# Performance work log

Measured on AMD Instinct MI355X. Metric: run time of the kernel, lower is better.

The kernel has to match this reference:

```python
import jax, jax.numpy as jnp
import numpy as np

N_EMBD = 1024
N_HEAD = 16

def setup_inputs() -> dict:
    key = jax.random.key(0)
    k1, k2, k3 = jax.random.split(key, 3)
    x = jax.random.normal(k1, (2, 2048, N_EMBD), dtype=jnp.float32)
    # torch Linear(n, 3n): y = x @ W_attn (we store transposed weight directly)
    w_attn = jax.random.normal(k2, (N_EMBD, 3 * N_EMBD), dtype=jnp.float32) * 0.02
    w_proj = jax.random.normal(k3, (N_EMBD, N_EMBD), dtype=jnp.float32) * 0.02
    return {"x": x, "w_attn": w_attn, "w_proj": w_proj}

def reference(x, w_attn, w_proj):
    B, S, E = x.shape
    H = N_HEAD
    D = E // H
    qkv = x @ w_attn  # [B, S, 3E]
    q, k, v = jnp.split(qkv, 3, axis=-1)
    # [B, H, S, D]
    q = q.reshape(B, S, H, D).transpose(0, 2, 1, 3)
    k = k.reshape(B, S, H, D).transpose(0, 2, 1, 3)
    v = v.reshape(B, S, H, D).transpose(0, 2, 1, 3)
    scale = 1.0 / jnp.sqrt(jnp.asarray(D, dtype=x.dtype))
    a = jnp.einsum('bhqd,bhkd->bhqk', q, k) * scale  # [B, H, S, S]
    causal = jnp.tril(jnp.ones((S, S), dtype=bool))
    a = jnp.where(causal, a, -jnp.inf)
    a = jax.nn.softmax(a, axis=-1)
    y = jnp.einsum('bhqk,bhkd->bhqd', a, v)  # [B, H, S, D]
    y = y.transpose(0, 2, 1, 3).reshape(B, S, E)
    return y @ w_proj
```

## Files before the change

### kernel.cpp

```cpp
#include <hip/hip_runtime.h>

#define DEVI __device__ __forceinline__

typedef short bf16x8 __attribute__((ext_vector_type(8)));
typedef float f32x4 __attribute__((ext_vector_type(4)));
typedef unsigned short u16;
typedef unsigned int u32;

static constexpr int Bn = 2, S = 2048, E = 1024, H = 16, D = 64;
static constexpr int Mrows = Bn * S;
static constexpr int N_QKV = 3 * E;

DEVI u16 f2b(float f) {
  union { float f; u32 u; } c; c.f = f;
  return (u16)((c.u + 0x7FFFu + ((c.u >> 16) & 1u)) >> 16);
}

DEVI bf16x8 ld8(const u16* p) {
  union { uint4 u; bf16x8 v; } c;
  c.u = *reinterpret_cast<const uint4*>(p);
  return c.v;
}

#define MFMA(a, b, c) __builtin_amdgcn_mfma_f32_16x16x32_bf16(a, b, c, 0, 0, 0)

#define G2L16(gptr, lptr) \
  __builtin_amdgcn_global_load_lds((const __attribute__((address_space(1))) void*)(gptr), \
                                   (__attribute__((address_space(3))) void*)(lptr), 16, 0, 0)

__global__ void conv_bf16(const float* __restrict__ in, u16* __restrict__ out, int n4) {
  int i = blockIdx.x * blockDim.x + threadIdx.x;
  if (i < n4) {
    float4 f = reinterpret_cast<const float4*>(in)[i];
    ushort4 u;
    u.x = f2b(f.x); u.y = f2b(f.y); u.z = f2b(f.z); u.w = f2b(f.w);
    reinterpret_cast<ushort4*>(out)[i] = u;
  }
}

__global__ void transpose_bf16(const float* __restrict__ in, u16* __restrict__ out, int R, int C) {
  __shared__ float t[32][33];
  int bx = blockIdx.x * 32;
  int by = blockIdx.y * 32;
  int tx = threadIdx.x, ty = threadIdx.y;
#pragma unroll
  for (int k = 0; k < 32; k += 8)
    t[ty + k][tx] = in[(size_t)(by + ty + k) * C + bx + tx];
  __syncthreads();
#pragma unroll
  for (int k = 0; k < 32; k += 8)
    out[(size_t)(bx + ty + k) * R + by + tx] = f2b(t[tx][ty + k]);
}

__global__ __launch_bounds__(256) void gemm_qkv(const u16* __restrict__ A, const u16* __restrict__ BT,
                                                u16* __restrict__ Qb, u16* __restrict__ Kb,
                                                u16* __restrict__ VbT) {
  constexpr int K = 1024, BK = 64;
  __shared__ __align__(16) u16 As[128 * BK];
  __shared__ __align__(16) u16 Bs[128 * BK];
  int tid = threadIdx.x;
  int w = tid >> 6, lane = tid & 63, quad = lane >> 4, l15 = lane & 15;
  int m0 = blockIdx.x * 128, n0 = blockIdx.y * 128;
  int mw = (w >> 1) * 64, nw = (w & 1) * 64;
  const u16* Ab = A + (size_t)m0 * K;
  const u16* Bb = BT + (size_t)n0 * K;
  f32x4 acc[4][4] = {};
  for (int k0 = 0; k0 < K; k0 += BK) {
#pragma unroll
    for (int j = 0; j < 4; j++) {
      int L = j * 256 + tid;
      int row = L >> 3, cg = (L & 7) ^ (row & 7);
      G2L16(Ab + (size_t)row * K + k0 + cg * 8, (char*)As + L * 16);
    }
#pragma unroll
    for (int j = 0; j < 4; j++) {
      int L = j * 256 + tid;
      int row = L >> 3, cg = (L & 7) ^ (row & 7);
      G2L16(Bb + (size_t)row * K + k0 + cg * 8, (char*)Bs + L * 16);
    }
    __syncthreads();
#pragma unroll
    for (int kk = 0; kk < 2; kk++) {
      int sg = ((kk << 2) | quad) ^ (l15 & 7);
      bf16x8 a[4], b[4];
#pragma unroll
      for (int i = 0; i < 4; i++) a[i] = ld8(&As[(mw + i * 16 + l15) * BK + sg * 8]);
#pragma unroll
      for (int i = 0; i < 4; i++) b[i] = ld8(&Bs[(nw + i * 16 + l15) * BK + sg * 8]);
#pragma unroll
      for (int mb = 0; mb < 4; mb++)
#pragma unroll
        for (int nb = 0; nb < 4; nb++)
          acc[mb][nb] = MFMA(a[mb], b[nb], acc[mb][nb]);
    }
    __syncthreads();
  }
#pragma unroll
  for (int mb = 0; mb < 4; mb++) {
    int m = m0 + mw + mb * 16 + quad * 4;
    int b = m >> 11, s = m & 2047;
#pragma unroll
    for (int nb = 0; nb < 4; nb++) {
      int n = n0 + nw + nb * 16 + l15;
      int sec = n >> 10, e = n & 1023, h = e >> 6, d = e & 63;
      int bh = b * H + h;
      if (sec == 0) {
#pragma unroll
        for (int r = 0; r < 4; r++)
          Qb[((size_t)bh * S + s + r) * D + d] = f2b(acc[mb][nb][r] * 0.125f);
      } else if (sec == 1) {
#pragma unroll
        for (int r = 0; r < 4; r++)
          Kb[((size_t)bh * S + s + r) * D + d] = f2b(acc[mb][nb][r]);
      } else {
        ushort4 v;
        v.x = f2b(acc[mb][nb][0]); v.y = f2b(acc[mb][nb][1]);
        v.z = f2b(acc[mb][nb][2]); v.w = f2b(acc[mb][nb][3]);
        *reinterpret_cast<ushort4*>(VbT + ((size_t)bh * D + d) * S + s) = v;
      }
    }
  }
}

__global__ __launch_bounds__(256, 3) void attn(const u16* __restrict__ Qb, const u16* __restrict__ Kb,
                                               const u16* __restrict__ VbT, u16* __restrict__ Yb) {
  __shared__ __align__(16) u16 Ks[128 * 64];
  __shared__ __align__(16) u16 Vs[64 * 128];
  __shared__ __align__(16) u32 Ps[4][16 * 68];
  int w = threadIdx.x >> 6, lane = threadIdx.x & 63, quad = lane >> 4, l15 = lane & 15;
  int bh = blockIdx.x & 31, p = blockIdx.x >> 5;
  int b = bh >> 4, h = bh & 15;

  const u16* Kbh = Kb + (size_t)bh * S * D;
  const u16* Vbh = VbT + (size_t)bh * D * S;
  u32* myP = &Ps[w][0];
  const u16* myP16 = (const u16*)myP;
  int prow = l15 * 68 + quad * 2;

#pragma unroll 1
  for (int ph = 0; ph < 2; ph++) {
    int qt = ph ? p : 31 - p;
    int q_base = qt * 64 + w * 16;
    int qrow = q_base + l15;
    int kmax = q_base + 16;
    int kend = (qt + 1) * 64;

    const u16* Qp = Qb + ((size_t)bh * S + qrow) * D + quad * 8;
    bf16x8 bq0 = ld8(Qp), bq1 = ld8(Qp + 32);

    float lpart = 0.f;
    f32x4 o[4] = {};

    for (int kbase = 0; kbase < kend; kbase += 128) {
      __syncthreads();
      const u16* Kg = Kbh + (size_t)kbase * D;
#pragma unroll
      for (int j = 0; j < 4; j++) {
        int L = (w * 4 + j) * 64 + lane;
        int row = L >> 3, cg = (L & 7) ^ (row & 7);
        G2L16(Kg + (size_t)row * 64 + cg * 8, (char*)Ks + L * 16);
      }
      const u16* Vg = Vbh + kbase;
#pragma unroll
      for (int j = 0; j < 4; j++) {
        int L = (w * 4 + j) * 64 + lane;
        int row = L >> 4, cg = (L & 15) ^ (row & 15);
        G2L16(Vg + (size_t)row * S + cg * 8, (char*)Vs + L * 16);
      }
      __syncthreads();

#pragma unroll
      for (int mb = 0; mb < 8; mb++) {
        int kb = kbase + mb * 16;
        u32 pa = 0, pb = 0;
        if (kb < kmax) {
          int row = mb * 16 + l15;
          bf16x8 ak0 = ld8(&Ks[row * 64 + ((quad ^ (row & 7)) * 8)]);
          bf16x8 ak1 = ld8(&Ks[row * 64 + (((quad + 4) ^ (row & 7)) * 8)]);
          f32x4 z = {};
          z = MFMA(ak0, bq0, z);
          z = MFMA(ak1, bq1, z);
          if (kb == q_base) {
#pragma unroll
            for (int r = 0; r < 4; r++)
              if (quad * 4 + r > l15) z[r] = -1e30f;
          }
          float p0 = __expf(z[0]), p1 = __expf(z[1]);
          float p2 = __expf(z[2]), p3 = __expf(z[3]);
          lpart += (p0 + p1) + (p2 + p3);
          pa = (u32)f2b(p0) | ((u32)f2b(p1) << 16);
          pb = (u32)f2b(p2) | ((u32)f2b(p3) << 16);
        }
        uint2 pw; pw.x = pa; pw.y = pb;
        *reinterpret_cast<uint2*>(&myP[prow + mb * 8]) = pw;
      }
#pragma unroll
      for (int ch = 0; ch < 4; ch++) {
        if (kbase + ch * 32 < kmax) {
          bf16x8 bp = ld8(myP16 + l15 * 136 + ch * 32 + quad * 8);
#pragma unroll
          for (int dd = 0; dd < 4; dd++) {
            int rv = dd * 16 + l15;
            bf16x8 av = ld8(&Vs[rv * 128 + (((ch * 4 + quad) ^ (rv & 15)) * 8)]);
            o[dd] = MFMA(av, bp, o[dd]);
          }
        }
      }
    }

    float l = lpart;
    l += __shfl_xor(l, 16);
    l += __shfl_xor(l, 32);
    float rinv = 1.0f / l;
    u16* Yp = Yb + ((size_t)b * S + qrow) * E + h * 64 + quad * 4;
#pragma unroll
    for (int dd = 0; dd < 4; dd++) {
      ushort4 y;
      y.x = f2b(o[dd][0] * rinv); y.y = f2b(o[dd][1] * rinv);
      y.z = f2b(o[dd][2] * rinv); y.w = f2b(o[dd][3] * rinv);
      *reinterpret_cast<ushort4*>(Yp + dd * 16) = y;
    }
  }
}

__global__ __launch_bounds__(256) void gemm_proj(const u16* __restrict__ A, const u16* __restrict__ BT,
                                                 float* __restrict__ out) {
  constexpr int K = 1024, BK = 64;
  __shared__ __align__(16) u16 As[128 * BK];
  __shared__ __align__(16) u16 Bs[128 * BK];
  int tid = threadIdx.x;
  int w = tid >> 6, lane = tid & 63, quad = lane >> 4, l15 = lane & 15;
  int m0 = blockIdx.x * 128, n0 = blockIdx.y * 128;
  int mw = (w >> 1) * 64, nw = (w & 1) * 64;
  const u16* Ab = A + (size_t)m0 * K;
  const u16* Bb = BT + (size_t)n0 * K;
  f32x4 acc[4][4] = {};
  for (int k0 = 0; k0 < K; k0 += BK) {
#pragma unroll
    for (int j = 0; j < 4; j++) {
      int L = j * 256 + tid;
      int row = L >> 3, cg = (L & 7) ^ (row & 7);
      G2L16(Ab + (size_t)row * K + k0 + cg * 8, (char*)As + L * 16);
    }
#pragma unroll
    for (int j = 0; j < 4; j++) {
      int L = j * 256 + tid;
      int row = L >> 3, cg = (L & 7) ^ (row & 7);
      G2L16(Bb + (size_t)row * K + k0 + cg * 8, (char*)Bs + L * 16);
    }
    __syncthreads();
#pragma unroll
    for (int kk = 0; kk < 2; kk++) {
      int sg = ((kk << 2) | quad) ^ (l15 & 7);
      bf16x8 a[4], b[4];
#pragma unroll
      for (int i = 0; i < 4; i++) a[i] = ld8(&As[(mw + i * 16 + l15) * BK + sg * 8]);
#pragma unroll
      for (int i = 0; i < 4; i++) b[i] = ld8(&Bs[(nw + i * 16 + l15) * BK + sg * 8]);
#pragma unroll
      for (int mb = 0; mb < 4; mb++)
#pragma unroll
        for (int nb = 0; nb < 4; nb++)
          acc[mb][nb] = MFMA(a[mb], b[nb], acc[mb][nb]);
    }
    __syncthreads();
  }
#pragma unroll
  for (int mb = 0; mb < 4; mb++) {
    int m = m0 + mw + mb * 16 + quad * 4;
#pragma unroll
    for (int nb = 0; nb < 4; nb++) {
      int n = n0 + nw + nb * 16 + l15;
#pragma unroll
      for (int r = 0; r < 4; r++)
        out[(size_t)(m + r) * E + n] = acc[mb][nb][r];
    }
  }
}

extern "C" void kernel_launch(void* const* d_in, const int* in_sizes, int n_in,
                              void* d_out, int out_size, void* d_ws, size_t ws_size,
                              hipStream_t stream) {
  const float* x = (const float*)d_in[0];
  const float* w_attn = (const float*)d_in[1];
  const float* w_proj = (const float*)d_in[2];
  float* out = (float*)d_out;
  char* ws = (char*)d_ws;

  u16* xb   = (u16*)(ws);
  u16* wabT = (u16*)(ws + 8388608);
  u16* wpbT = (u16*)(ws + 14680064);
  u16* Qb   = (u16*)(ws + 16777216);
  u16* Kb   = (u16*)(ws + 25165824);
  u16* VbT  = (u16*)(ws + 33554432);
  u16* Yb   = (u16*)(ws + 41943040);

  conv_bf16<<<4096, 256, 0, stream>>>(x, xb, Mrows * E / 4);
  transpose_bf16<<<dim3(N_QKV / 32, E / 32), dim3(32, 8), 0, stream>>>(w_attn, wabT, E, N_QKV);
  transpose_bf16<<<dim3(E / 32, E / 32), dim3(32, 8), 0, stream>>>(w_proj, wpbT, E, E);
  gemm_qkv<<<dim3(Mrows / 128, N_QKV / 128), 256, 0, stream>>>(xb, wabT, Qb, Kb, VbT);
  attn<<<Bn * H * (S / 128), 256, 0, stream>>>(Qb, Kb, VbT, Yb);
  gemm_proj<<<dim3(Mrows / 128, E / 128), 256, 0, stream>>>(Yb, wpbT, out);
}
```

Measured before the change: 188.7 us.

## Load GEMM B operand directly from global and fuse paired attention query tiles

```diff
diff --git a/kernel.cpp b/kernel.cpp
--- a/kernel.cpp
+++ b/kernel.cpp
@@ -55,38 +55,32 @@
 __global__ __launch_bounds__(256) void gemm_qkv(const u16* __restrict__ A, const u16* __restrict__ BT,
                                                 u16* __restrict__ Qb, u16* __restrict__ Kb,
                                                 u16* __restrict__ VbT) {
-  constexpr int K = 1024, BK = 64;
+  constexpr int K = 1024, BK = 128;
   __shared__ __align__(16) u16 As[128 * BK];
-  __shared__ __align__(16) u16 Bs[128 * BK];
   int tid = threadIdx.x;
   int w = tid >> 6, lane = tid & 63, quad = lane >> 4, l15 = lane & 15;
   int m0 = blockIdx.x * 128, n0 = blockIdx.y * 128;
   int mw = (w >> 1) * 64, nw = (w & 1) * 64;
   const u16* Ab = A + (size_t)m0 * K;
-  const u16* Bb = BT + (size_t)n0 * K;
+  const u16* Bp = BT + (size_t)(n0 + nw + l15) * K + quad * 8;
   f32x4 acc[4][4] = {};
   for (int k0 = 0; k0 < K; k0 += BK) {
 #pragma unroll
-    for (int j = 0; j < 4; j++) {
+    for (int j = 0; j < 8; j++) {
       int L = j * 256 + tid;
-      int row = L >> 3, cg = (L & 7) ^ (row & 7);
+      int row = L >> 4, cg = (L & 15) ^ (row & 15);
       G2L16(Ab + (size_t)row * K + k0 + cg * 8, (char*)As + L * 16);
     }
-#pragma unroll
-    for (int j = 0; j < 4; j++) {
-      int L = j * 256 + tid;
-      int row = L >> 3, cg = (L & 7) ^ (row & 7);
-      G2L16(Bb + (size_t)row * K + k0 + cg * 8, (char*)Bs + L * 16);
-    }
-    __syncthreads();
-#pragma unroll
-    for (int kk = 0; kk < 2; kk++) {
-      int sg = ((kk << 2) | quad) ^ (l15 & 7);
-      bf16x8 a[4], b[4];
-#pragma unroll
-      for (int i = 0; i < 4; i++) a[i] = ld8(&As[(mw + i * 16 + l15) * BK + sg * 8]);
-#pragma unroll
-      for (int i = 0; i < 4; i++) b[i] = ld8(&Bs[(nw + i * 16 + l15) * BK + sg * 8]);
+    __syncthreads();
+#pragma unroll
+    for (int kk = 0; kk < 4; kk++) {
+      bf16x8 b[4];
+#pragma unroll
+      for (int nb = 0; nb < 4; nb++) b[nb] = ld8(Bp + (size_t)nb * 16 * K + k0 + kk * 32);
+      bf16x8 a[4];
+#pragma unroll
+      for (int i = 0; i < 4; i++)
+        a[i] = ld8(&As[(mw + i * 16 + l15) * BK + ((((kk << 2) | quad) ^ l15) * 8)]);
 #pragma unroll
       for (int mb = 0; mb < 4; mb++)
 #pragma unroll
@@ -130,6 +124,8 @@
   int w = threadIdx.x >> 6, lane = threadIdx.x & 63, quad = lane >> 4, l15 = lane & 15;
   int bh = blockIdx.x & 31, p = blockIdx.x >> 5;
   int b = bh >> 4, h = bh & 15;
+  int qtA = 31 - p, qtB = p;
+  int ncA = (qtA + 2) >> 1, ncB = (qtB + 2) >> 1;
 
   const u16* Kbh = Kb + (size_t)bh * S * D;
   const u16* Vbh = VbT + (size_t)bh * D * S;
@@ -137,87 +133,102 @@
   const u16* myP16 = (const u16*)myP;
   int prow = l15 * 68 + quad * 2;
 
-#pragma unroll 1
-  for (int ph = 0; ph < 2; ph++) {
-    int qt = ph ? p : 31 - p;
-    int q_base = qt * 64 + w * 16;
-    int qrow = q_base + l15;
-    int kmax = q_base + 16;
-    int kend = (qt + 1) * 64;
-
-    const u16* Qp = Qb + ((size_t)bh * S + qrow) * D + quad * 8;
-    bf16x8 bq0 = ld8(Qp), bq1 = ld8(Qp + 32);
-
-    float lpart = 0.f;
-    f32x4 o[4] = {};
-
-    for (int kbase = 0; kbase < kend; kbase += 128) {
-      __syncthreads();
-      const u16* Kg = Kbh + (size_t)kbase * D;
-#pragma unroll
-      for (int j = 0; j < 4; j++) {
-        int L = (w * 4 + j) * 64 + lane;
-        int row = L >> 3, cg = (L & 7) ^ (row & 7);
-        G2L16(Kg + (size_t)row * 64 + cg * 8, (char*)Ks + L * 16);
+  int qbA = qtA * 64 + w * 16, qbB = qtB * 64 + w * 16;
+  int kmaxA = qbA + 16, kmaxB = qbB + 16;
+  const u16* QpA = Qb + ((size_t)bh * S + qbA + l15) * D + quad * 8;
+  const u16* QpB = Qb + ((size_t)bh * S + qbB + l15) * D + quad * 8;
+  bf16x8 bqA0 = ld8(QpA), bqA1 = ld8(QpA + 32);
+  bf16x8 bqB0 = ld8(QpB), bqB1 = ld8(QpB + 32);
+
+  float lA = 0.f, lB = 0.f;
+  f32x4 oA[4] = {}, oB[4] = {};
+  int kbase = 0;
+
+  auto process = [&](int q_base, int kmaxW, bf16x8 bq0, bf16x8 bq1, f32x4* o, float& lpart) {
+#pragma unroll
+    for (int mb = 0; mb < 8; mb++) {
+      int kb = kbase + mb * 16;
+      u32 pa = 0, pb = 0;
+      if (kb < kmaxW) {
+        int row = mb * 16 + l15;
+        bf16x8 ak0 = ld8(&Ks[row * 64 + ((quad ^ (row & 7)) * 8)]);
+        bf16x8 ak1 = ld8(&Ks[row * 64 + (((quad + 4) ^ (row & 7)) * 8)]);
+        f32x4 z = {};
+        z = MFMA(ak0, bq0, z);
+        z = MFMA(ak1, bq1, z);
+        if (kb == q_base) {
+#pragma unroll
+          for (int r = 0; r < 4; r++)
+            if (quad * 4 + r > l15) z[r] = -1e30f;
+        }
+        float p0 = __expf(z[0]), p1 = __expf(z[1]);
+        float p2 = __expf(z[2]), p3 = __expf(z[3]);
+        lpart += (p0 + p1) + (p2 + p3);
+        pa = (u32)f2b(p0) | ((u32)f2b(p1) << 16);
+        pb = (u32)f2b(p2) | ((u32)f2b(p3) << 16);
       }
-      const u16* Vg = Vbh + kbase;
-#pragma unroll
-      for (int j = 0; j < 4; j++) {
-        int L = (w * 4 + j) * 64 + lane;
-        int row = L >> 4, cg = (L & 15) ^ (row & 15);
-        G2L16(Vg + (size_t)row * S + cg * 8, (char*)Vs + L * 16);
-      }
-      __syncthreads();
-
-#pragma unroll
-      for (int mb = 0; mb < 8; mb++) {
-        int kb = kbase + mb * 16;
-        u32 pa = 0, pb = 0;
-        if (kb < kmax) {
-          int row = mb * 16 + l15;
-          bf16x8 ak0 = ld8(&Ks[row * 64 + ((quad ^ (row & 7)) * 8)]);
-          bf16x8 ak1 = ld8(&Ks[row * 64 + (((quad + 4) ^ (row & 7)) * 8)]);
-          f32x4 z = {};
-          z = MFMA(ak0, bq0, z);
-          z = MFMA(ak1, bq1, z);
-          if (kb == q_base) {
-#pragma unroll
-            for (int r = 0; r < 4; r++)
-              if (quad * 4 + r > l15) z[r] = -1e30f;
-          }
-          float p0 = __expf(z[0]), p1 = __expf(z[1]);
-          float p2 = __expf(z[2]), p3 = __expf(z[3]);
-          lpart += (p0 + p1) + (p2 + p3);
-          pa = (u32)f2b(p0) | ((u32)f2b(p1) << 16);
-          pb = (u32)f2b(p2) | ((u32)f2b(p3) << 16);
-        }
-        uint2 pw; pw.x = pa; pw.y = pb;
-        *reinterpret_cast<uint2*>(&myP[prow + mb * 8]) = pw;
-      }
-#pragma unroll
-      for (int ch = 0; ch < 4; ch++) {
-        if (kbase + ch * 32 < kmax) {
-          bf16x8 bp = ld8(myP16 + l15 * 136 + ch * 32 + quad * 8);
-#pragma unroll
-          for (int dd = 0; dd < 4; dd++) {
-            int rv = dd * 16 + l15;
-            bf16x8 av = ld8(&Vs[rv * 128 + (((ch * 4 + quad) ^ (rv & 15)) * 8)]);
-            o[dd] = MFMA(av, bp, o[dd]);
-          }
+      uint2 pw; pw.x = pa; pw.y = pb;
+      *reinterpret_cast<uint2*>(&myP[prow + mb * 8]) = pw;
+    }
+#pragma unroll
+    for (int ch = 0; ch < 4; ch++) {
+      if (kbase + ch * 32 < kmaxW) {
+        bf16x8 bp = ld8(myP16 + l15 * 136 + ch * 32 + quad * 8);
+#pragma unroll
+        for (int dd = 0; dd < 4; dd++) {
+          int rv = dd * 16 + l15;
+          bf16x8 av = ld8(&Vs[rv * 128 + (((ch * 4 + quad) ^ (rv & 15)) * 8)]);
+          o[dd] = MFMA(av, bp, o[dd]);
         }
       }
     }
-
-    float l = lpart;
-    l += __shfl_xor(l, 16);
-    l += __shfl_xor(l, 32);
+  };
+
+  for (int c = 0; c < ncA; c++) {
+    kbase = c * 128;
+    __syncthreads();
+    const u16* Kg = Kbh + (size_t)kbase * D;
+#pragma unroll
+    for (int j = 0; j < 4; j++) {
+      int L = (w * 4 + j) * 64 + lane;
+      int row = L >> 3, cg = (L & 7) ^ (row & 7);
+      G2L16(Kg + (size_t)row * 64 + cg * 8, (char*)Ks + L * 16);
+    }
+    const u16* Vg = Vbh + kbase;
+#pragma unroll
+    for (int j = 0; j < 4; j++) {
+      int L = (w * 4 + j) * 64 + lane;
+      int row = L >> 4, cg = (L & 15) ^ (row & 15);
+      G2L16(Vg + (size_t)row * S + cg * 8, (char*)Vs + L * 16);
+    }
+    __syncthreads();
+
+    process(qbA, kmaxA, bqA0, bqA1, oA, lA);
+    if (c < ncB)
+      process(qbB, kmaxB, bqB0, bqB1, oB, lB);
+  }
+
+  {
+    float l = lA; l += __shfl_xor(l, 16); l += __shfl_xor(l, 32);
     float rinv = 1.0f / l;
-    u16* Yp = Yb + ((size_t)b * S + qrow) * E + h * 64 + quad * 4;
+    u16* Yp = Yb + ((size_t)b * S + qbA + l15) * E + h * 64 + quad * 4;
 #pragma unroll
     for (int dd = 0; dd < 4; dd++) {
       ushort4 y;
-      y.x = f2b(o[dd][0] * rinv); y.y = f2b(o[dd][1] * rinv);
-      y.z = f2b(o[dd][2] * rinv); y.w = f2b(o[dd][3] * rinv);
+      y.x = f2b(oA[dd][0] * rinv); y.y = f2b(oA[dd][1] * rinv);
+      y.z = f2b(oA[dd][2] * rinv); y.w = f2b(oA[dd][3] * rinv);
+      *reinterpret_cast<ushort4*>(Yp + dd * 16) = y;
+    }
+  }
+  {
+    float l = lB; l += __shfl_xor(l, 16); l += __shfl_xor(l, 32);
+    float rinv = 1.0f / l;
+    u16* Yp = Yb + ((size_t)b * S + qbB + l15) * E + h * 64 + quad * 4;
+#pragma unroll
+    for (int dd = 0; dd < 4; dd++) {
+      ushort4 y;
+      y.x = f2b(oB[dd][0] * rinv); y.y = f2b(oB[dd][1] * rinv);
+      y.z = f2b(oB[dd][2] * rinv); y.w = f2b(oB[dd][3] * rinv);
       *reinterpret_cast<ushort4*>(Yp + dd * 16) = y;
     }
   }
@@ -225,38 +236,32 @@
 
 __global__ __launch_bounds__(256) void gemm_proj(const u16* __restrict__ A, const u16* __restrict__ BT,
                                                  float* __restrict__ out) {
-  constexpr int K = 1024, BK = 64;
+  constexpr int K = 1024, BK = 128;
   __shared__ __align__(16) u16 As[128 * BK];
-  __shared__ __align__(16) u16 Bs[128 * BK];
   int tid = threadIdx.x;
   int w = tid >> 6, lane = tid & 63, quad = lane >> 4, l15 = lane & 15;
   int m0 = blockIdx.x * 128, n0 = blockIdx.y * 128;
   int mw = (w >> 1) * 64, nw = (w & 1) * 64;
   const u16* Ab = A + (size_t)m0 * K;
-  const u16* Bb = BT + (size_t)n0 * K;
+  const u16* Bp = BT + (size_t)(n0 + nw + l15) * K + quad * 8;
   f32x4 acc[4][4] = {};
   for (int k0 = 0; k0 < K; k0 += BK) {
 #pragma unroll
-    for (int j = 0; j < 4; j++) {
+    for (int j = 0; j < 8; j++) {
       int L = j * 256 + tid;
-      int row = L >> 3, cg = (L & 7) ^ (row & 7);
+      int row = L >> 4, cg = (L & 15) ^ (row & 15);
       G2L16(Ab + (size_t)row * K + k0 + cg * 8, (char*)As + L * 16);
     }
-#pragma unroll
-    for (int j = 0; j < 4; j++) {
-      int L = j * 256 + tid;
-      int row = L >> 3, cg = (L & 7) ^ (row & 7);
-      G2L16(Bb + (size_t)row * K + k0 + cg * 8, (char*)Bs + L * 16);
-    }
-    __syncthreads();
-#pragma unroll
-    for (int kk = 0; kk < 2; kk++) {
-      int sg = ((kk << 2) | quad) ^ (l15 & 7);
-      bf16x8 a[4], b[4];
-#pragma unroll
-      for (int i = 0; i < 4; i++) a[i] = ld8(&As[(mw + i * 16 + l15) * BK + sg * 8]);
-#pragma unroll
-      for (int i = 0; i < 4; i++) b[i] = ld8(&Bs[(nw + i * 16 + l15) * BK + sg * 8]);
+    __syncthreads();
+#pragma unroll
+    for (int kk = 0; kk < 4; kk++) {
+      bf16x8 b[4];
+#pragma unroll
+      for (int nb = 0; nb < 4; nb++) b[nb] = ld8(Bp + (size_t)nb * 16 * K + k0 + kk * 32);
+      bf16x8 a[4];
+#pragma unroll
+      for (int i = 0; i < 4; i++)
+        a[i] = ld8(&As[(mw + i * 16 + l15) * BK + ((((kk << 2) | quad) ^ l15) * 8)]);
 #pragma unroll
       for (int mb = 0; mb < 4; mb++)
 #pragma unroll
```

Result: slower. 213.8 us (+13.3%).
